# Performance work log

Measured on AMD Instinct MI355X. Metric: run time of the kernel, lower is better.

Reference implementation:

```python
import jax, jax.numpy as jnp
import numpy as np
from jax import lax

B, CIN, H, W = 16, 128, 56, 56
COUT, K, STRIDE, PAD, DIL = 256, 3, 1, 1, 1
D = 8  # lattice.d
KE = K * K
M = CIN * KE // D  # sub-vectors per spatial position


def setup_inputs() -> dict:
    key = jax.random.key(0)
    k1, k2, k3 = jax.random.split(key, 3)
    input_encodings = jax.random.normal(k1, (B, CIN, H, W), dtype=jnp.float32)
    weight_encodings = jax.random.normal(k2, (COUT, M, D), dtype=jnp.float32)
    bias = jax.random.normal(k3, (COUT,), dtype=jnp.float32)
    return {"input_encodings": input_encodings,
            "weight_encodings": weight_encodings,
            "bias": bias}


def reference(input_encodings, weight_encodings, bias):
    b, cin, h, w = input_encodings.shape
    cout, m, d = weight_encodings.shape
    h_out = (h + 2 * PAD - DIL * (K - 1) - 1) // STRIDE + 1
    w_out = (w + 2 * PAD - DIL * (K - 1) - 1) // STRIDE + 1
    L = h_out * w_out
    # im2col / unfold: (B, Cin*K*K, Hout, Wout), channel-major (c, kh, kw) ordering
    patches = lax.conv_general_dilated_patches(
        input_encodings, (K, K), (STRIDE, STRIDE), [(PAD, PAD), (PAD, PAD)],
        rhs_dilation=(DIL, DIL))
    # (B, L, M, D): each position split into M lattice-encoded sub-vectors of dim D
    x = patches.reshape(b, cin * K * K, L).transpose(0, 2, 1).reshape(b, L, m, d)
    # two-sided vLUT matrix multiply == sum of per-sub-vector inner products
    out = jnp.einsum('blmd,omd->bol', x, weight_encodings)  # (B, Cout, L)
    out = out.reshape(b, cout, h_out, w_out)
    return out + bias[None, :, None, None]
```

## Files before the change

kernel.cpp:

```cpp
#include <hip/hip_runtime.h>
#include <hip/hip_bf16.h>

#define CIN_   128
#define HW_    56
#define LHW_   3136
#define COUT_  256
#define KTOT_  1152
#define TH_    2
#define SPT_   112
#define NF_    7
#define SCOLS_ 58
#define SPP_   232
#define CSTR_  128

typedef unsigned short u16;
typedef __attribute__((ext_vector_type(8))) short short8v;
typedef __attribute__((ext_vector_type(4))) float f32x4;

__device__ __forceinline__ u16 f2bf(float f) {
  union { float f; unsigned u; } v; v.f = f;
  unsigned u = v.u;
  u += 0x7fffu + ((u >> 16) & 1u);
  return (u16)(u >> 16);
}
__device__ __forceinline__ unsigned pack2(u16 a, u16 b) {
  return (unsigned)a | ((unsigned)b << 16);
}

__global__ void wreorder2_kernel(const float* __restrict__ w, u16* __restrict__ wb,
                                 u16* __restrict__ zp) {
  if (blockIdx.x == 0 && threadIdx.x < 16) {
    uint4 z; z.x = z.y = z.z = z.w = 0u;
    reinterpret_cast<uint4*>(zp)[threadIdx.x] = z;
  }
  int j = blockIdx.x * 256 + threadIdx.x;
  int c4 = j & 31;
  int o  = (j >> 5) & 255;
  int t  = j >> 13;
  int c0i = c4 >> 3;
  int lg  = (c4 >> 1) & 3;
  size_t slot = ((size_t)(t * 4 + c0i) * 16 + (o >> 4)) * 64 + lg * 16 + (o & 15);
  const float* src = w + (size_t)o * KTOT_ + t;
  ushort4 r;
  r.x = f2bf(src[(c4 * 4 + 0) * 9]);
  r.y = f2bf(src[(c4 * 4 + 1) * 9]);
  r.z = f2bf(src[(c4 * 4 + 2) * 9]);
  r.w = f2bf(src[(c4 * 4 + 3) * 9]);
  *reinterpret_cast<ushort4*>(wb + slot * 8 + (c4 & 1) * 4) = r;
}

__global__ void wreorder_kernel(const float* __restrict__ w, u16* __restrict__ wb) {
  int j = blockIdx.x * 256 + threadIdx.x;
  int c4 = j & 31;
  int o  = (j >> 5) & 255;
  int t  = j >> 13;
  const float* src = w + (size_t)o * KTOT_ + t;
  ushort4 r;
  r.x = f2bf(src[(c4 * 4 + 0) * 9]);
  r.y = f2bf(src[(c4 * 4 + 1) * 9]);
  r.z = f2bf(src[(c4 * 4 + 2) * 9]);
  r.w = f2bf(src[(c4 * 4 + 3) * 9]);
  *reinterpret_cast<ushort4*>(wb + ((size_t)(t * 256 + o) * CSTR_ + c4 * 4)) = r;
}

#define TLDSW_ 136
__global__ __launch_bounds__(256) void nhwc_kernel(
    const float* __restrict__ in, u16* __restrict__ xin) {
  __shared__ u16 ts[64 * TLDSW_];
  const int bp = blockIdx.x;
  const int b = bp / 49;
  const int pos0 = (bp % 49) * 64;
  const int tid = threadIdx.x;
  const float* ib = in + (size_t)b * CIN_ * LHW_ + pos0;
  {
    const int p  = tid & 63;
    const int c0 = (tid >> 6) * 32;
    #pragma unroll
    for (int i = 0; i < 32; ++i)
      ts[p * TLDSW_ + c0 + i] = f2bf(ib[(size_t)(c0 + i) * LHW_ + p]);
  }
  __syncthreads();
  {
    const int p  = tid >> 2;
    const int c0 = (tid & 3) * 32;
    u16* dst = xin + ((size_t)b * LHW_ + pos0 + p) * CIN_ + c0;
    const u16* srcr = &ts[p * TLDSW_ + c0];
    #pragma unroll
    for (int j = 0; j < 4; ++j)
      reinterpret_cast<uint4*>(dst)[j] =
          *reinterpret_cast<const uint4*>(srcr + j * 8);
  }
}

__device__ __forceinline__ void gload_lds16(const void* g, void* l) {
  __builtin_amdgcn_global_load_lds(
      (const __attribute__((address_space(1))) void*)g,
      (__attribute__((address_space(3))) void*)l, 16, 0, 0);
}

__global__ __launch_bounds__(256, 2) void conv5_kernel(
    const u16* __restrict__ xin, const u16* __restrict__ wb2,
    const float* __restrict__ bias, const u16* __restrict__ zpage,
    float* __restrict__ out)
{
  __shared__ u16 xs[SPP_ * CSTR_];

  const int tid  = threadIdx.x;
  const int lane = tid & 63;
  const int wc   = tid >> 6;
  const int lr   = lane & 15;
  const int lg   = lane >> 4;
  const int lg8  = lg * 8;

  const int swz = (blockIdx.x & 7) * 56 + (blockIdx.x >> 3);
  const int b   = swz / 28;
  const int ty  = swz % 28;
  const int iy0 = ty * TH_ - 1;

  const u16* xb = xin + (size_t)b * LHW_ * CIN_;

  #pragma unroll
  for (int i = 0; i < 15; ++i) {
    int idx = i * 256 + tid;
    if (idx < SPP_ * 16) {
      int spp   = idx >> 4;
      int chunk = idx & 15;
      int rr = spp / SCOLS_;
      int cc = spp - rr * SCOLS_;
      int iy = iy0 + rr;
      int ix = cc - 1;
      int sch = chunk ^ (spp & 7);
      const u16* src =
          ((unsigned)iy < (unsigned)HW_ && (unsigned)ix < (unsigned)HW_)
              ? xb + ((size_t)(iy * HW_ + ix) * CIN_ + sch * 8)
              : zpage;
      u16* ldst = xs + (size_t)(idx & ~63) * 8;
      gload_lds16(src, ldst);
    }
  }

  int spp0[NF_];
  #pragma unroll
  for (int nf = 0; nf < NF_; ++nf) {
    int sp = nf * 16 + lr;
    int r  = (sp >= 56) ? 1 : 0;
    int x  = sp - r * 56;
    spp0[nf] = (r + 1) * SCOLS_ + (x + 1);
  }

  f32x4 acc[4][NF_];
  #pragma unroll
  for (int m = 0; m < 4; ++m)
    #pragma unroll
    for (int nf = 0; nf < NF_; ++nf)
      acc[m][nf] = f32x4{0.f, 0.f, 0.f, 0.f};

  __syncthreads();

  const short8v* pA = reinterpret_cast<const short8v*>(wb2);

  auto loadA = [&](int t4c, short8v* dst) {
    const short8v* p = pA + ((size_t)t4c * 16 + wc * 4) * 64 + lane;
    #pragma unroll
    for (int ai = 0; ai < 4; ++ai) dst[ai] = p[ai * 64];
  };
  auto loadB = [&](int dspp, int c0, short8v* dst) {
    #pragma unroll
    for (int nf = 0; nf < NF_; ++nf) {
      int spp = spp0[nf] + dspp;
      int off = (spp << 7) + ((c0 + lg8) ^ ((spp & 7) << 3));
      dst[nf] = *reinterpret_cast<const short8v*>(&xs[off]);
    }
  };

  short8v A0[4], A1[4], B0[NF_], B1[NF_];

#define MFMA_GRP(Ab, Bb)                                                        \
  {                                                                             \
    __builtin_amdgcn_s_setprio(1);                                              \
    _Pragma("unroll")                                                           \
    for (int ai = 0; ai < 4; ++ai) {                                            \
      _Pragma("unroll")                                                         \
      for (int nf = 0; nf < NF_; ++nf)                                          \
        acc[ai][nf] = __builtin_amdgcn_mfma_f32_16x16x32_bf16(                  \
            (Ab)[ai], (Bb)[nf], acc[ai][nf], 0, 0, 0);                          \
    }                                                                           \
    __builtin_amdgcn_s_setprio(0);                                              \
  }

  loadA(0, A0);
  loadB(-SCOLS_ - 1, 0, B0);

  #pragma unroll 1
  for (int t = 0; t < 9; ++t) {
    const int dty  = t / 3;
    const int dspp = (dty - 1) * SCOLS_ + (t - 3 * dty) - 1;
    const int t4   = t * 4;

    loadA(t4 + 1, A1); loadB(dspp, 32, B1);
    MFMA_GRP(A0, B0);
    loadA(t4 + 2, A0); loadB(dspp, 64, B0);
    MFMA_GRP(A1, B1);
    loadA(t4 + 3, A1); loadB(dspp, 96, B1);
    MFMA_GRP(A0, B0);
    if (t < 8) {
      const int tn   = t + 1;
      const int ndty = tn / 3;
      const int nds  = (ndty - 1) * SCOLS_ + (tn - 3 * ndty) - 1;
      loadA(t4 + 4, A0); loadB(nds, 0, B0);
    }
    MFMA_GRP(A1, B1);
  }

  float* ob = out + (size_t)b * COUT_ * LHW_ + ty * SPT_;
  const int obase = wc * 64 + lg * 4;
  #pragma unroll
  for (int ai = 0; ai < 4; ++ai) {
    #pragma unroll
    for (int rr = 0; rr < 4; ++rr) {
      const int o = obase + ai * 16 + rr;
      const float bs = bias[o];
      #pragma unroll
      for (int nf = 0; nf < NF_; ++nf)
        ob[(size_t)o * LHW_ + nf * 16 + lr] = acc[ai][nf][rr] + bs;
    }
  }
#undef MFMA_GRP
}

__global__ __launch_bounds__(256, 2) void conv2_kernel(
    const float* __restrict__ in, const u16* __restrict__ wb,
    const float* __restrict__ bias, float* __restrict__ out)
{
  __shared__ u16 xs[SPP_ * CSTR_];
  const int tid  = threadIdx.x;
  const int lane = tid & 63;
  const int wid  = tid >> 6;
  const int lr   = lane & 15;
  const int lg   = lane >> 4;
  const int bid = blockIdx.x;
  const int ch  = bid & 1;
  const int ty  = (bid >> 1) % 28;
  const int b   = bid / 56;
  const float* inb = in + (size_t)b * CIN_ * LHW_;
  const int iy0 = ty * TH_ - 1;

  #pragma unroll 1
  for (int i = 0; i < 15; ++i) {
    int idx = i * 256 + tid;
    if (idx < SPP_ * 16) {
      int cg  = idx / SPP_;
      int spp = idx - cg * SPP_;
      int rr  = spp / SCOLS_;
      int cc  = spp - rr * SCOLS_;
      int iy  = iy0 + rr;
      int ix  = cc - 1;
      bool ok = ((unsigned)iy < (unsigned)HW_) && ((unsigned)ix < (unsigned)HW_);
      const float* p = inb + (size_t)cg * 8 * LHW_ + iy * HW_ + ix;
      u16 v[8];
      #pragma unroll
      for (int jj = 0; jj < 8; ++jj)
        v[jj] = f2bf(ok ? p[jj * LHW_] : 0.f);
      uint4 pk;
      pk.x = pack2(v[0], v[1]); pk.y = pack2(v[2], v[3]);
      pk.z = pack2(v[4], v[5]); pk.w = pack2(v[6], v[7]);
      *reinterpret_cast<uint4*>(&xs[spp * CSTR_ + ((cg * 8) ^ ((spp & 7) << 3))]) = pk;
    }
  }
  int spp0[NF_];
  #pragma unroll
  for (int nf = 0; nf < NF_; ++nf) {
    int sp = nf * 16 + lr;
    int r  = (sp >= 56) ? 1 : 0;
    int x  = sp - r * 56;
    spp0[nf] = (r + 1) * SCOLS_ + x + 1;
  }
  f32x4 acc[2][NF_];
  #pragma unroll
  for (int m = 0; m < 2; ++m)
    #pragma unroll
    for (int nf = 0; nf < NF_; ++nf)
      acc[m][nf] = f32x4{0.f, 0.f, 0.f, 0.f};
  __syncthreads();
  const u16* wt0 = wb + (size_t)(ch * 128 + wid * 32 + lr) * CSTR_ + lg * 8;
  #pragma unroll 1
  for (int t = 0; t < 9; ++t) {
    const int dspp = (t / 3 - 1) * SCOLS_ + (t % 3 - 1);
    const u16* wt = wt0 + (size_t)t * 256 * CSTR_;
    #pragma unroll
    for (int c0i = 0; c0i < 4; ++c0i) {
      const int c0 = c0i * 32;
      short8v a0 = *reinterpret_cast<const short8v*>(wt + c0);
      short8v a1 = *reinterpret_cast<const short8v*>(wt + 16 * CSTR_ + c0);
      short8v bv[NF_];
      #pragma unroll
      for (int nf = 0; nf < NF_; ++nf) {
        int spp = spp0[nf] + dspp;
        int off = spp * CSTR_ + ((c0 + lg * 8) ^ ((spp & 7) << 3));
        bv[nf] = *reinterpret_cast<const short8v*>(&xs[off]);
      }
      #pragma unroll
      for (int nf = 0; nf < NF_; ++nf) {
        acc[0][nf] = __builtin_amdgcn_mfma_f32_16x16x32_bf16(a0, bv[nf], acc[0][nf], 0, 0, 0);
        acc[1][nf] = __builtin_amdgcn_mfma_f32_16x16x32_bf16(a1, bv[nf], acc[1][nf], 0, 0, 0);
      }
    }
  }
  float* ob = out + (size_t)b * COUT_ * LHW_ + ty * SPT_;
  const int obase = ch * 128 + wid * 32 + lg * 4;
  #pragma unroll
  for (int m = 0; m < 2; ++m)
    #pragma unroll
    for (int rr = 0; rr < 4; ++rr) {
      const int o = obase + m * 16 + rr;
      const float bs = bias[o];
      #pragma unroll
      for (int nf = 0; nf < NF_; ++nf)
        ob[(size_t)o * LHW_ + nf * 16 + lr] = acc[m][nf][rr] + bs;
    }
}

#define SPT0_  64
#define BK0_   32
#define NKS0_  36
#define LDSW0_ 40
__global__ __launch_bounds__(256, 2) void conv_fb_kernel(
    const float* __restrict__ in, const float* __restrict__ wf,
    const float* __restrict__ bias, float* __restrict__ out)
{
  __shared__ u16 xs[SPT0_ * LDSW0_];
  const int tid = threadIdx.x;
  const int lane = tid & 63;
  const int wid = tid >> 6;
  const int lg = lane >> 4;
  const int lr = lane & 15;
  const int bid = blockIdx.x;
  const int b = bid / 49;
  const int l0 = (bid % 49) * SPT0_;
  const int sp = tid & 63;
  const int qq = tid >> 6;
  const int l = l0 + sp;
  const int y = l / HW_;
  const int x = l - y * HW_;
  const float* inb = in + (size_t)b * CIN_ * LHW_;
  f32x4 acc[4][4];
  #pragma unroll
  for (int i = 0; i < 4; ++i)
    #pragma unroll
    for (int j = 0; j < 4; ++j) acc[i][j] = f32x4{0.f, 0.f, 0.f, 0.f};
  auto stage_load = [&](int ks) -> uint4 {
    int kbase = ks * BK0_ + qq * 8;
    int c = kbase / 9;
    int t = kbase - c * 9;
    u16 v[8];
    #pragma unroll
    for (int j = 0; j < 8; ++j) {
      int dy = (t * 11) >> 5;
      int dx = t - 3 * dy;
      int yy = y + dy - 1, xx = x + dx - 1;
      float f = 0.f;
      if ((unsigned)yy < (unsigned)HW_ && (unsigned)xx < (unsigned)HW_)
        f = inb[(c * HW_ + yy) * HW_ + xx];
      v[j] = f2bf(f);
      ++t; if (t == 9) { t = 0; ++c; }
    }
    uint4 r;
    r.x = pack2(v[0], v[1]); r.y = pack2(v[2], v[3]);
    r.z = pack2(v[4], v[5]); r.w = pack2(v[6], v[7]);
    return r;
  };
  uint4 st = stage_load(0);
  for (int ks = 0; ks < NKS0_; ++ks) {
    __syncthreads();
    *reinterpret_cast<uint4*>(&xs[sp * LDSW0_ + qq * 8]) = st;
    __syncthreads();
    if (ks + 1 < NKS0_) st = stage_load(ks + 1);
    const int k0 = ks * BK0_;
    short8v a[4];
    #pragma unroll
    for (int ai = 0; ai < 4; ++ai) {
      const int o = wid * 64 + ai * 16 + lr;
      const float* p = wf + (size_t)o * KTOT_ + k0 + lg * 8;
      u16 t8[8];
      #pragma unroll
      for (int j = 0; j < 8; ++j) t8[j] = f2bf(p[j]);
      union { uint4 u; short8v s; } cv;
      cv.u.x = pack2(t8[0], t8[1]); cv.u.y = pack2(t8[2], t8[3]);
      cv.u.z = pack2(t8[4], t8[5]); cv.u.w = pack2(t8[6], t8[7]);
      a[ai] = cv.s;
    }
    short8v bv[4];
    #pragma unroll
    for (int sj = 0; sj < 4; ++sj)
      bv[sj] = *reinterpret_cast<const short8v*>(&xs[(sj * 16 + lr) * LDSW0_ + lg * 8]);
    #pragma unroll
    for (int ai = 0; ai < 4; ++ai)
      #pragma unroll
      for (int sj = 0; sj < 4; ++sj)
        acc[ai][sj] = __builtin_amdgcn_mfma_f32_16x16x32_bf16(a[ai], bv[sj], acc[ai][sj], 0, 0, 0);
  }
  float* outb = out + (size_t)b * COUT_ * LHW_ + l0;
  #pragma unroll
  for (int ai = 0; ai < 4; ++ai)
    #pragma unroll
    for (int r = 0; r < 4; ++r) {
      const int o = wid * 64 + ai * 16 + lg * 4 + r;
      const float bvs = bias[o];
      #pragma unroll
      for (int sj = 0; sj < 4; ++sj)
        outb[(size_t)o * LHW_ + sj * 16 + lr] = acc[ai][sj][r] + bvs;
    }
}

extern "C" void kernel_launch(void* const* d_in, const int* in_sizes, int n_in,
                              void* d_out, int out_size, void* d_ws, size_t ws_size,
                              hipStream_t stream) {
  (void)in_sizes; (void)n_in; (void)out_size;
  const float* in   = (const float*)d_in[0];
  const float* w    = (const float*)d_in[1];
  const float* bias = (const float*)d_in[2];
  float* out = (float*)d_out;

  const size_t wbytes  = (size_t)COUT_ * KTOT_ * sizeof(u16);
  const size_t xbytes  = (size_t)16 * LHW_ * CIN_ * sizeof(u16);
  const size_t need    = wbytes + xbytes + 256;

  if (ws_size >= need) {
    u16* wb2 = (u16*)d_ws;
    u16* xin = wb2 + wbytes / 2;
    u16* zp  = xin + xbytes / 2;
    wreorder2_kernel<<<dim3(288), dim3(256), 0, stream>>>(w, wb2, zp);
    nhwc_kernel<<<dim3(784), dim3(256), 0, stream>>>(in, xin);
    conv5_kernel<<<dim3(448), dim3(256), 0, stream>>>(xin, wb2, bias, zp, out);
  } else if (ws_size >= wbytes) {
    u16* wb = (u16*)d_ws;
    wreorder_kernel<<<dim3(288), dim3(256), 0, stream>>>(w, wb);
    conv2_kernel<<<dim3(896), dim3(256), 0, stream>>>(in, wb, bias, out);
  } else {
    conv_fb_kernel<<<dim3(784), dim3(256), 0, stream>>>(in, w, bias, out);
  }
}
```

Before: 67.27 us.

## Replace halo-tile conv kernel with double-buffered implicit-GEMM streaming A and B through LDS

Replaces the conv5 kernel, which kept a 2-row input halo tile in LDS and read weights straight from global into registers, with conv6. Conv6 tiles the output as 128 channels by 128 flattened positions and walks 36 K-steps, double-buffering both the weight slice and the gathered input slice in LDS via global_load_lds. The aim is higher occupancy (launch bounds 3, smaller LDS) and overlap of loads with MFMA across 784 blocks. In exchange, the halo reuse is lost: each input element is re-fetched for all 9 taps, and every K-step ends in a barrier.

```diff
diff --git a/kernel.cpp b/kernel.cpp
--- a/kernel.cpp
+++ b/kernel.cpp
@@ -6,12 +6,6 @@
 #define LHW_   3136
 #define COUT_  256
 #define KTOT_  1152
-#define TH_    2
-#define SPT_   112
-#define NF_    7
-#define SCOLS_ 58
-#define SPP_   232
-#define CSTR_  128
 
 typedef unsigned short u16;
 typedef __attribute__((ext_vector_type(8))) short short8v;
@@ -60,7 +54,7 @@
   r.y = f2bf(src[(c4 * 4 + 1) * 9]);
   r.z = f2bf(src[(c4 * 4 + 2) * 9]);
   r.w = f2bf(src[(c4 * 4 + 3) * 9]);
-  *reinterpret_cast<ushort4*>(wb + ((size_t)(t * 256 + o) * CSTR_ + c4 * 4)) = r;
+  *reinterpret_cast<ushort4*>(wb + ((size_t)(t * 256 + o) * 128 + c4 * 4)) = r;
 }
 
 #define TLDSW_ 136
@@ -98,136 +92,113 @@
       (__attribute__((address_space(3))) void*)l, 16, 0, 0);
 }
 
-__global__ __launch_bounds__(256, 2) void conv5_kernel(
+__global__ __launch_bounds__(256, 3) void conv6_kernel(
     const u16* __restrict__ xin, const u16* __restrict__ wb2,
     const float* __restrict__ bias, const u16* __restrict__ zpage,
     float* __restrict__ out)
 {
-  __shared__ u16 xs[SPP_ * CSTR_];
+  __shared__ __align__(16) u16 alds[2][4096];
+  __shared__ __align__(16) u16 blds[2][4096];
 
   const int tid  = threadIdx.x;
   const int lane = tid & 63;
-  const int wc   = tid >> 6;
+  const int wid  = tid >> 6;
+  const int wc   = wid & 1;
+  const int ws   = wid >> 1;
   const int lr   = lane & 15;
   const int lg   = lane >> 4;
-  const int lg8  = lg * 8;
-
-  const int swz = (blockIdx.x & 7) * 56 + (blockIdx.x >> 3);
-  const int b   = swz / 28;
-  const int ty  = swz % 28;
-  const int iy0 = ty * TH_ - 1;
-
-  const u16* xb = xin + (size_t)b * LHW_ * CIN_;
-
-  #pragma unroll
-  for (int i = 0; i < 15; ++i) {
-    int idx = i * 256 + tid;
-    if (idx < SPP_ * 16) {
-      int spp   = idx >> 4;
-      int chunk = idx & 15;
-      int rr = spp / SCOLS_;
-      int cc = spp - rr * SCOLS_;
-      int iy = iy0 + rr;
-      int ix = cc - 1;
-      int sch = chunk ^ (spp & 7);
-      const u16* src =
-          ((unsigned)iy < (unsigned)HW_ && (unsigned)ix < (unsigned)HW_)
-              ? xb + ((size_t)(iy * HW_ + ix) * CIN_ + sch * 8)
-              : zpage;
-      u16* ldst = xs + (size_t)(idx & ~63) * 8;
-      gload_lds16(src, ldst);
-    }
-  }
-
-  int spp0[NF_];
-  #pragma unroll
-  for (int nf = 0; nf < NF_; ++nf) {
-    int sp = nf * 16 + lr;
-    int r  = (sp >= 56) ? 1 : 0;
-    int x  = sp - r * 56;
-    spp0[nf] = (r + 1) * SCOLS_ + (x + 1);
-  }
-
-  f32x4 acc[4][NF_];
-  #pragma unroll
-  for (int m = 0; m < 4; ++m)
-    #pragma unroll
-    for (int nf = 0; nf < NF_; ++nf)
-      acc[m][nf] = f32x4{0.f, 0.f, 0.f, 0.f};
-
+
+  const int g   = (blockIdx.x & 7) * 98 + (blockIdx.x >> 3);
+  const int coh = g & 1;
+  const int nt  = g >> 1;
+
+  const int p   = tid & 127;
+  const int lgi = tid >> 7;
+  const int n   = nt * 128 + p;
+  const int bb  = n / LHW_;
+  const int ll  = n - bb * LHW_;
+  const int py  = ll / HW_;
+  const int px  = ll - py * HW_;
+  const u16* bsrc0 = xin + (size_t)n * CIN_ + lgi * 8;
+
+  auto stage = [&](int ks, int h) {
+    {
+      const u16* s0 = wb2 + ((size_t)ks * 1024 + coh * 512 + tid) * 8;
+      gload_lds16(s0,        &alds[h][(size_t)(tid & ~63) * 8]);
+      gload_lds16(s0 + 2048, &alds[h][(size_t)((tid + 256) & ~63) * 8]);
+    }
+    {
+      const int t   = ks >> 2;
+      const int c0i = ks & 3;
+      const int dy  = t / 3;
+      const int dx  = t - dy * 3;
+      const int yy  = py + dy - 1;
+      const int xx  = px + dx - 1;
+      const bool ok = ((unsigned)yy < (unsigned)HW_) & ((unsigned)xx < (unsigned)HW_);
+      const u16* sB  = ok ? bsrc0 + ((dy - 1) * HW_ + (dx - 1)) * CIN_ + c0i * 32
+                          : zpage;
+      const u16* sB1 = ok ? sB + 16 : zpage;
+      gload_lds16(sB,  &blds[h][(size_t)(tid & ~63) * 8]);
+      gload_lds16(sB1, &blds[h][(size_t)((tid + 256) & ~63) * 8]);
+    }
+  };
+
+  f32x4 acc[4][4];
+  #pragma unroll
+  for (int i = 0; i < 4; ++i)
+    #pragma unroll
+    for (int j = 0; j < 4; ++j)
+      acc[i][j] = f32x4{0.f, 0.f, 0.f, 0.f};
+
+  stage(0, 0);
   __syncthreads();
 
-  const short8v* pA = reinterpret_cast<const short8v*>(wb2);
-
-  auto loadA = [&](int t4c, short8v* dst) {
-    const short8v* p = pA + ((size_t)t4c * 16 + wc * 4) * 64 + lane;
-    #pragma unroll
-    for (int ai = 0; ai < 4; ++ai) dst[ai] = p[ai * 64];
-  };
-  auto loadB = [&](int dspp, int c0, short8v* dst) {
-    #pragma unroll
-    for (int nf = 0; nf < NF_; ++nf) {
-      int spp = spp0[nf] + dspp;
-      int off = (spp << 7) + ((c0 + lg8) ^ ((spp & 7) << 3));
-      dst[nf] = *reinterpret_cast<const short8v*>(&xs[off]);
-    }
-  };
-
-  short8v A0[4], A1[4], B0[NF_], B1[NF_];
-
-#define MFMA_GRP(Ab, Bb)                                                        \
-  {                                                                             \
-    __builtin_amdgcn_s_setprio(1);                                              \
-    _Pragma("unroll")                                                           \
-    for (int ai = 0; ai < 4; ++ai) {                                            \
-      _Pragma("unroll")                                                         \
-      for (int nf = 0; nf < NF_; ++nf)                                          \
-        acc[ai][nf] = __builtin_amdgcn_mfma_f32_16x16x32_bf16(                  \
-            (Ab)[ai], (Bb)[nf], acc[ai][nf], 0, 0, 0);                          \
-    }                                                                           \
-    __builtin_amdgcn_s_setprio(0);                                              \
-  }
-
-  loadA(0, A0);
-  loadB(-SCOLS_ - 1, 0, B0);
-
   #pragma unroll 1
-  for (int t = 0; t < 9; ++t) {
-    const int dty  = t / 3;
-    const int dspp = (dty - 1) * SCOLS_ + (t - 3 * dty) - 1;
-    const int t4   = t * 4;
-
-    loadA(t4 + 1, A1); loadB(dspp, 32, B1);
-    MFMA_GRP(A0, B0);
-    loadA(t4 + 2, A0); loadB(dspp, 64, B0);
-    MFMA_GRP(A1, B1);
-    loadA(t4 + 3, A1); loadB(dspp, 96, B1);
-    MFMA_GRP(A0, B0);
-    if (t < 8) {
-      const int tn   = t + 1;
-      const int ndty = tn / 3;
-      const int nds  = (ndty - 1) * SCOLS_ + (tn - 3 * ndty) - 1;
-      loadA(t4 + 4, A0); loadB(nds, 0, B0);
-    }
-    MFMA_GRP(A1, B1);
-  }
-
-  float* ob = out + (size_t)b * COUT_ * LHW_ + ty * SPT_;
-  const int obase = wc * 64 + lg * 4;
-  #pragma unroll
-  for (int ai = 0; ai < 4; ++ai) {
-    #pragma unroll
-    for (int rr = 0; rr < 4; ++rr) {
-      const int o = obase + ai * 16 + rr;
-      const float bs = bias[o];
-      #pragma unroll
-      for (int nf = 0; nf < NF_; ++nf)
-        ob[(size_t)o * LHW_ + nf * 16 + lr] = acc[ai][nf][rr] + bs;
-    }
-  }
-#undef MFMA_GRP
-}
-
+  for (int ks = 0; ks < 36; ++ks) {
+    const int h = ks & 1;
+    if (ks < 35) stage(ks + 1, h ^ 1);
+
+    short8v a[4], b[4];
+    #pragma unroll
+    for (int ai = 0; ai < 4; ++ai)
+      a[ai] = *reinterpret_cast<const short8v*>(
+          &alds[h][(size_t)((wc * 4 + ai) * 64 + lg * 16 + lr) * 8]);
+    #pragma unroll
+    for (int nj = 0; nj < 4; ++nj)
+      b[nj] = *reinterpret_cast<const short8v*>(
+          &blds[h][(size_t)(lg * 128 + ws * 64 + nj * 16 + lr) * 8]);
+
+    #pragma unroll
+    for (int ai = 0; ai < 4; ++ai)
+      #pragma unroll
+      for (int nj = 0; nj < 4; ++nj)
+        acc[ai][nj] = __builtin_amdgcn_mfma_f32_16x16x32_bf16(
+            a[ai], b[nj], acc[ai][nj], 0, 0, 0);
+
+    __syncthreads();
+  }
+
+  #pragma unroll
+  for (int nj = 0; nj < 4; ++nj) {
+    const int nb0 = nt * 128 + ws * 64 + nj * 16;
+    const int ob  = nb0 / LHW_;
+    const int ol  = nb0 - ob * LHW_;
+    float* obp = out + (size_t)ob * COUT_ * LHW_ + ol + lr;
+    #pragma unroll
+    for (int ai = 0; ai < 4; ++ai) {
+      #pragma unroll
+      for (int rr = 0; rr < 4; ++rr) {
+        const int o = coh * 128 + wc * 64 + ai * 16 + lg * 4 + rr;
+        obp[(size_t)o * LHW_] = acc[ai][nj][rr] + bias[o];
+      }
+    }
+  }
+}
+
+#define NF_    7
+#define SCOLS_ 58
+#define SPP_   232
+#define CSTR_  128
 __global__ __launch_bounds__(256, 2) void conv2_kernel(
     const float* __restrict__ in, const u16* __restrict__ wb,
     const float* __restrict__ bias, float* __restrict__ out)
@@ -243,7 +214,7 @@
   const int ty  = (bid >> 1) % 28;
   const int b   = bid / 56;
   const float* inb = in + (size_t)b * CIN_ * LHW_;
-  const int iy0 = ty * TH_ - 1;
+  const int iy0 = ty * 2 - 1;
 
   #pragma unroll 1
   for (int i = 0; i < 15; ++i) {
@@ -256,11 +227,11 @@
       int iy  = iy0 + rr;
       int ix  = cc - 1;
       bool ok = ((unsigned)iy < (unsigned)HW_) && ((unsigned)ix < (unsigned)HW_);
-      const float* p = inb + (size_t)cg * 8 * LHW_ + iy * HW_ + ix;
+      const float* pp = inb + (size_t)cg * 8 * LHW_ + iy * HW_ + ix;
       u16 v[8];
       #pragma unroll
       for (int jj = 0; jj < 8; ++jj)
-        v[jj] = f2bf(ok ? p[jj * LHW_] : 0.f);
+        v[jj] = f2bf(ok ? pp[jj * LHW_] : 0.f);
       uint4 pk;
       pk.x = pack2(v[0], v[1]); pk.y = pack2(v[2], v[3]);
       pk.z = pack2(v[4], v[5]); pk.w = pack2(v[6], v[7]);
@@ -306,7 +277,7 @@
       }
     }
   }
-  float* ob = out + (size_t)b * COUT_ * LHW_ + ty * SPT_;
+  float* ob = out + (size_t)b * COUT_ * LHW_ + ty * 112;
   const int obase = ch * 128 + wid * 32 + lg * 4;
   #pragma unroll
   for (int m = 0; m < 2; ++m)
@@ -380,10 +351,10 @@
     #pragma unroll
     for (int ai = 0; ai < 4; ++ai) {
       const int o = wid * 64 + ai * 16 + lr;
-      const float* p = wf + (size_t)o * KTOT_ + k0 + lg * 8;
+      const float* pp = wf + (size_t)o * KTOT_ + k0 + lg * 8;
       u16 t8[8];
       #pragma unroll
-      for (int j = 0; j < 8; ++j) t8[j] = f2bf(p[j]);
+      for (int j = 0; j < 8; ++j) t8[j] = f2bf(pp[j]);
       union { uint4 u; short8v s; } cv;
       cv.u.x = pack2(t8[0], t8[1]); cv.u.y = pack2(t8[2], t8[3]);
       cv.u.z = pack2(t8[4], t8[5]); cv.u.w = pack2(t8[6], t8[7]);
@@ -431,7 +402,7 @@
     u16* zp  = xin + xbytes / 2;
     wreorder2_kernel<<<dim3(288), dim3(256), 0, stream>>>(w, wb2, zp);
     nhwc_kernel<<<dim3(784), dim3(256), 0, stream>>>(in, xin);
-    conv5_kernel<<<dim3(448), dim3(256), 0, stream>>>(xin, wb2, bias, zp, out);
+    conv6_kernel<<<dim3(784), dim3(256), 0, stream>>>(xin, wb2, bias, zp, out);
   } else if (ws_size >= wbytes) {
     u16* wb = (u16*)d_ws;
     wreorder_kernel<<<dim3(288), dim3(256), 0, stream>>>(w, wb);
```

New measurement: 70.03 us. 4.1% more time.
